# Performance work log

Measured on AMD Instinct MI355X. Metric: run time of the kernel, lower is better.

Reference implementation:

```python
import jax, jax.numpy as jnp
import numpy as np
from jax import lax

B, T, N, H, NC = 2, 8, 512, 64, 10
NEG = -1e9
LN_EPS = 1e-5


def _gatv2(x, mask, Wl, Wr, att, b):
    # GATv2Conv (PyG semantics, eval mode): e_ij = att . leaky_relu(Wr x_i + Wl x_j),
    # softmax over source nodes j with self-loops, out_i = sum_j alpha_ij * (Wl x_j).
    # x: (B, N, Fin); mask: (N, N) bool adjacency incl. self-loops; att: (heads, C).
    heads, C = att.shape
    Bn, Nn, _ = x.shape
    xl = (x @ Wl).reshape(Bn, Nn, heads, C)  # source transform
    xr = (x @ Wr).reshape(Bn, Nn, heads, C)  # target transform
    s = jax.nn.leaky_relu(xr[:, :, None] + xl[:, None, :], 0.2)  # (B, Ni, Nj, h, C)
    e = jnp.einsum('bijhc,hc->bijh', s, att)
    e = jnp.where(mask[None, :, :, None], e, NEG)
    alpha = jax.nn.softmax(e, axis=2)  # softmax over neighbors j
    out = jnp.einsum('bijh,bjhc->bihc', alpha, xl)
    return out.reshape(Bn, Nn, heads * C) + b


def _gru_layer(x, Wih, Whh, bih, bhh):
    # torch nn.GRU single layer, batch_first; x: (B, T, Hin)
    h0 = jnp.zeros((x.shape[0], Whh.shape[0]), x.dtype)
    def step(h, xt):
        gi = xt @ Wih + bih
        gh = h @ Whh + bhh
        ir, iz, inn = jnp.split(gi, 3, axis=-1)
        hr, hz, hn = jnp.split(gh, 3, axis=-1)
        r = jax.nn.sigmoid(ir + hr)
        z = jax.nn.sigmoid(iz + hz)
        n = jnp.tanh(inn + r * hn)
        hnew = (1.0 - z) * n + z * h
        return hnew, hnew
    _, ys = lax.scan(step, h0, jnp.swapaxes(x, 0, 1))
    return jnp.swapaxes(ys, 0, 1)


def setup_inputs() -> dict:
    key = jax.random.key(0)
    ks = jax.random.split(key, 20)
    def rn(i, shape, s=0.1):
        return jax.random.normal(ks[i], shape, jnp.float32) * s
    x_seq = jax.random.normal(ks[0], (B, T, N, 1), jnp.float32)
    a = jax.random.uniform(ks[1], (N, N))
    up = jnp.triu((a > 0.95).astype(jnp.float32), 1)
    static_adj = up + up.T  # sparse symmetric 0/1 static graph
    dyn_W = jax.random.normal(ks[2], (N, N), jnp.float32)
    reg_lambda = jnp.array([0.05], jnp.float32)
    return {
        'x_seq': x_seq, 'static_adj': static_adj, 'dyn_W': dyn_W, 'reg_lambda': reg_lambda,
        'g1_Wl': rn(3, (1, H)), 'g1_Wr': rn(4, (1, H)), 'g1_att': rn(5, (4, H // 4)), 'g1_b': jnp.zeros(H),
        'g2_Wl': rn(6, (H, H)), 'g2_Wr': rn(7, (H, H)), 'g2_att': rn(8, (1, H)), 'g2_b': jnp.zeros(H),
        'gru_Wih0': rn(9, (H, 3 * H)), 'gru_Whh0': rn(10, (H, 3 * H)), 'gru_bih0': jnp.zeros(3 * H), 'gru_bhh0': jnp.zeros(3 * H),
        'gru_Wih1': rn(11, (H, 3 * H)), 'gru_Whh1': rn(12, (H, 3 * H)), 'gru_bih1': jnp.zeros(3 * H), 'gru_bhh1': jnp.zeros(3 * H),
        'attn_W': rn(13, (H, 1)), 'attn_b': jnp.zeros(1),
        'cls_W1': rn(14, (H, H)), 'cls_b1': jnp.zeros(H), 'ln_g': jnp.ones(H), 'ln_b': jnp.zeros(H),
        'cls_W2': rn(15, (H, NC)), 'cls_b2': jnp.zeros(NC),
    }


def reference(x_seq, static_adj, dyn_W, reg_lambda,
              g1_Wl, g1_Wr, g1_att, g1_b, g2_Wl, g2_Wr, g2_att, g2_b,
              gru_Wih0, gru_Whh0, gru_bih0, gru_bhh0,
              gru_Wih1, gru_Whh1, gru_bih1, gru_bhh1,
              attn_W, attn_b, cls_W1, cls_b1, ln_g, ln_b, cls_W2, cls_b2):
    Bn, Tn, Nn, _ = x_seq.shape
    lam = jnp.maximum(reg_lambda[0], 0.01)
    t = jnp.arange(Tn, dtype=x_seq.dtype)
    gts = jnp.exp(-lam * t)  # gating values per timestep
    dyn = jax.nn.relu(dyn_W + dyn_W.T)
    fused = gts[:, None, None] * static_adj + (1.0 - gts)[:, None, None] * dyn  # (T, N, N)
    masks = (fused > 0) | jnp.eye(Nn, dtype=bool)[None]  # edge set + self-loops

    def step(carry, inp):
        xt, mask = inp  # xt: (B, N, 1)
        h = jax.nn.elu(_gatv2(xt, mask, g1_Wl, g1_Wr, g1_att, g1_b))
        h = jax.nn.elu(_gatv2(h, mask, g2_Wl, g2_Wr, g2_att, g2_b))
        return carry, h.mean(axis=1)  # (B, H) graph readout

    _, reps = lax.scan(step, 0.0, (jnp.swapaxes(x_seq, 0, 1), masks))
    h_seq = jnp.swapaxes(reps, 0, 1)  # (B, T, H)

    gru_out = _gru_layer(h_seq, gru_Wih0, gru_Whh0, gru_bih0, gru_bhh0)
    gru_out = _gru_layer(gru_out, gru_Wih1, gru_Whh1, gru_bih1, gru_bhh1)

    att_scores = jax.nn.softmax((gru_out @ attn_W + attn_b)[..., 0], axis=1)  # (B, T)
    final = jnp.einsum('bt,bth->bh', att_scores, gru_out)

    z = final @ cls_W1 + cls_b1
    mu = jnp.mean(z, axis=-1, keepdims=True)
    var = jnp.var(z, axis=-1, keepdims=True)
    z = (z - mu) / jnp.sqrt(var + LN_EPS) * ln_g + ln_b
    z = jax.nn.gelu(z, approximate=False)
    logits = z @ cls_W2 + cls_b2
    return logits, gts, att_scores
```

## Files before the change

### kernel.cpp

```cpp
#include <hip/hip_runtime.h>
#include <math.h>

#define BB 2
#define TT 8
#define NN 512
#define HH 64
#define NC 10

typedef unsigned char uchar;

__device__ __forceinline__ float elu1(float v){ return v > 0.f ? v : expm1f(v); }
__device__ __forceinline__ float sigm(float v){ return 1.f/(1.f+expf(-v)); }

__global__ __launch_bounds__(256) void k_mask(
    const float* __restrict__ dW, const float* __restrict__ sadj,
    uchar* __restrict__ M0, uchar* __restrict__ M1,
    float* __restrict__ hseq,
    const float* __restrict__ att1, const float* __restrict__ Wr1,
    const float* __restrict__ Wl1, float* __restrict__ AB,
    const float* __restrict__ Whh0, const float* __restrict__ Wih1,
    const float* __restrict__ Whh1, float4* __restrict__ WT4)
{
    __shared__ float tr[64][65];
    int bx = blockIdx.x, by = blockIdx.y;
    int tid = threadIdx.x;
    if (blockIdx.z == 1){
        int idx = (by*8 + bx)*256 + tid;
        if (idx < 3*4096){
            int m = idx >> 12, r = idx & 4095;
            int gg = r >> 6, k = r & 63;
            const float* W = (m == 0) ? Whh0 : (m == 1) ? Wih1 : Whh1;
            float4 o;
            o.x = W[k*192 + gg];
            o.y = W[k*192 + 64 + gg];
            o.z = W[k*192 + 128 + gg];
            o.w = 0.f;
            WT4[(size_t)m*4096 + r] = o;
        }
        return;
    }
    int i0 = by*64, j0 = bx*64;
    #pragma unroll
    for (int q = 0; q < 4; ++q){
        int r = (tid >> 4) + 16*q, c4 = tid & 15;
        float4 v = *(const float4*)&dW[(size_t)(j0+r)*NN + i0 + 4*c4];
        tr[r][4*c4+0] = v.x; tr[r][4*c4+1] = v.y;
        tr[r][4*c4+2] = v.z; tr[r][4*c4+3] = v.w;
    }
    __syncthreads();
    #pragma unroll
    for (int q = 0; q < 4; ++q){
        int row = (tid >> 4) + 16*q, c4 = tid & 15;
        int i = i0 + row, j = j0 + 4*c4;
        float4 d  = *(const float4*)&dW[(size_t)i*NN + j];
        float4 sa = *(const float4*)&sadj[(size_t)i*NN + j];
        uchar4 m0, m1;
        float dd0 = d.x + tr[4*c4+0][row];
        float dd1 = d.y + tr[4*c4+1][row];
        float dd2 = d.z + tr[4*c4+2][row];
        float dd3 = d.w + tr[4*c4+3][row];
        m0.x = (sa.x > 0.f) || (i == j+0);
        m0.y = (sa.y > 0.f) || (i == j+1);
        m0.z = (sa.z > 0.f) || (i == j+2);
        m0.w = (sa.w > 0.f) || (i == j+3);
        m1.x = m0.x || (dd0 > 0.f);
        m1.y = m0.y || (dd1 > 0.f);
        m1.z = m0.z || (dd2 > 0.f);
        m1.w = m0.w || (dd3 > 0.f);
        *(uchar4*)&M0[(size_t)i*NN + j] = m0;
        *(uchar4*)&M1[(size_t)i*NN + j] = m1;
    }
    int flat = (by*8 + bx)*256 + tid;
    if (flat < BB*TT*HH) hseq[flat] = 0.f;
    if (bx == 0 && by == 0 && tid < 8){
        int h = tid & 3;
        const float* W = (tid < 4) ? Wr1 : Wl1;
        float s = 0.f;
        for (int c = 0; c < 16; ++c) s += att1[h*16+c]*W[h*16+c];
        AB[tid] = s;
    }
}

__global__ __launch_bounds__(256) void k_gat1f(
    const float* __restrict__ x_seq, const uchar* __restrict__ M0,
    const uchar* __restrict__ M1,
    const float* __restrict__ Wl, const float* __restrict__ Wr,
    const float* __restrict__ att, const float* __restrict__ bias,
    const float* __restrict__ AB,
    const float* __restrict__ Wl2, const float* __restrict__ Wr2,
    const float* __restrict__ att2,
    float* __restrict__ xl2, float* __restrict__ xr2,
    float* __restrict__ ui, float* __restrict__ vj)
{
    __shared__ float x_s[NN];
    __shared__ float S_s[4][4];
    __shared__ float h_s[4][HH];
    __shared__ float Wl2_s[64*64];
    __shared__ float Wr2_s[64*64];
    int bt = blockIdx.y; int t = bt % TT;
    int i0 = blockIdx.x * 4;
    int tid = threadIdx.x;
    int il = tid >> 6, jl = tid & 63;
    int i = i0 + il;
    const uchar* M = t ? M1 : M0;
    ((float2*)x_s)[tid] = ((const float2*)(x_seq + bt*NN))[tid];
    #pragma unroll
    for (int q = 0; q < 4; ++q){
        int idx = q*256 + tid;
        ((float4*)Wl2_s)[idx] = ((const float4*)Wl2)[idx];
        ((float4*)Wr2_s)[idx] = ((const float4*)Wr2)[idx];
    }
    __syncthreads();
    float xi = x_s[i];
    const uchar* Mrow = M + (size_t)i*NN;
    float xj[8], msk[8];
    #pragma unroll
    for (int jj = 0; jj < 8; ++jj){
        int j = jj*64 + jl;
        xj[jj] = x_s[j];
        msk[jj] = Mrow[j] ? 1.f : 0.f;
    }
    float sw[4] = {0,0,0,0}, swx[4] = {0,0,0,0};
    for (int h = 0; h < 4; ++h){
        float acc[8] = {0,0,0,0,0,0,0,0};
        #pragma unroll
        for (int c = 0; c < 16; ++c){
            int hc = h*16 + c;
            float wl = Wl[hc];
            float q  = 0.4f * att[hc];
            float pr = xi * Wr[hc];
            #pragma unroll
            for (int jj = 0; jj < 8; ++jj){
                float s = fmaf(xj[jj], wl, pr);
                acc[jj] = fmaf(q, fabsf(s), acc[jj]);
            }
        }
        float lin = 0.6f * xi * AB[h];
        float al6 = 0.6f * AB[4+h];
        #pragma unroll
        for (int jj = 0; jj < 8; ++jj){
            float e = acc[jj] + fmaf(al6, xj[jj], lin);
            float w = msk[jj] * __expf(e);
            sw[h] += w;
            swx[h] = fmaf(w, xj[jj], swx[h]);
        }
    }
    #pragma unroll
    for (int off = 32; off; off >>= 1){
        #pragma unroll
        for (int h = 0; h < 4; ++h){
            sw[h]  += __shfl_down(sw[h],  off);
            swx[h] += __shfl_down(swx[h], off);
        }
    }
    if (jl == 0){
        #pragma unroll
        for (int h = 0; h < 4; ++h) S_s[il][h] = swx[h] / sw[h];
    }
    __syncthreads();
    {
        int hc = tid & 63, row = tid >> 6;
        float v = S_s[row][hc >> 4] * Wl[hc] + bias[hc];
        h_s[row][hc] = elu1(v);
    }
    __syncthreads();
    {
        int c = tid & 63, row = tid >> 6;
        float al = 0.f, ar = 0.f;
        #pragma unroll 8
        for (int k = 0; k < 64; ++k){
            float hv = h_s[row][k];
            al = fmaf(hv, Wl2_s[k*64 + c], al);
            ar = fmaf(hv, Wr2_s[k*64 + c], ar);
        }
        size_t ridx = (size_t)(bt*NN + i0 + row);
        xl2[ridx*HH + c] = al;
        xr2[ridx*HH + c] = ar;
        float a2 = att2[c];
        float pu = a2 * ar, pv = a2 * al;
        #pragma unroll
        for (int off = 32; off; off >>= 1){
            pu += __shfl_down(pu, off);
            pv += __shfl_down(pv, off);
        }
        if (c == 0){ ui[ridx] = pu; vj[ridx] = pv; }
    }
}

__global__ __launch_bounds__(256) void k_gat2(
    const float* __restrict__ xl2, const float* __restrict__ xr2,
    const uchar* __restrict__ M0, const uchar* __restrict__ M1,
    const float* __restrict__ att, const float* __restrict__ ui,
    const float* __restrict__ vj, const float* __restrict__ bias,
    float* __restrict__ hseq)
{
    __shared__ float xl_s[128][68];
    __shared__ float wT_s[128][36];
    __shared__ float xrT_s[64][36];
    __shared__ float v_s[128];
    __shared__ float u_s[32];
    __shared__ float z_s[32];
    __shared__ float q_s[64];

    int bt = blockIdx.y, t = bt & 7;
    int i0 = blockIdx.x * 32;
    int base = bt * NN;
    int tid = threadIdx.x;
    const uchar* M = t ? M1 : M0;

    #pragma unroll
    for (int q = 0; q < 2; ++q){
        int idx = q*256 + tid;
        int row = idx >> 4, c4 = idx & 15;
        float4 xv = ((const float4*)&xr2[(size_t)(base+i0+row)*HH])[c4];
        xrT_s[c4*4+0][row] = xv.x;
        xrT_s[c4*4+1][row] = xv.y;
        xrT_s[c4*4+2][row] = xv.z;
        xrT_s[c4*4+3][row] = xv.w;
    }
    if (tid < 32) u_s[tid] = ui[base + i0 + tid];
    if (tid < 64) q_s[tid] = 0.4f * att[tid];

    int ig = tid >> 5, jg = tid & 31;
    int wv = tid >> 6, ln = tid & 63;
    int ig2 = ln >> 3, cg2 = ln & 7;

    float zreg[4] = {0.f,0.f,0.f,0.f};
    float acc[4][8];
    #pragma unroll
    for (int a = 0; a < 4; ++a)
        #pragma unroll
        for (int r = 0; r < 8; ++r) acc[a][r] = 0.f;

    for (int tile = 0; tile < 4; ++tile){
        int j0 = tile * 128;
        __syncthreads();
        #pragma unroll
        for (int q = 0; q < 8; ++q){
            int idx = q*256 + tid;
            int row = idx >> 4, c4 = idx & 15;
            ((float4*)&xl_s[row][0])[c4] = ((const float4*)&xl2[(size_t)(base+j0+row)*HH])[c4];
        }
        if (tid < 128) v_s[tid] = vj[base + j0 + tid];
        __syncthreads();
        float e[4][4];
        {
            float u0 = 0.6f*u_s[ig*4+0], u1 = 0.6f*u_s[ig*4+1];
            float u2 = 0.6f*u_s[ig*4+2], u3 = 0.6f*u_s[ig*4+3];
            #pragma unroll
            for (int jj = 0; jj < 4; ++jj){
                float vv = 0.6f * v_s[jj*32 + jg];
                e[0][jj] = u0 + vv; e[1][jj] = u1 + vv;
                e[2][jj] = u2 + vv; e[3][jj] = u3 + vv;
            }
        }
        #pragma unroll 4
        for (int c4 = 0; c4 < 16; ++c4){
            float q4[4], xr4[4][4], xl4[4][4];
            *(float4*)q4 = *(const float4*)&q_s[c4*4];
            #pragma unroll
            for (int k = 0; k < 4; ++k)
                *(float4*)xr4[k] = *(const float4*)&xrT_s[c4*4+k][ig*4];
            #pragma unroll
            for (int jj = 0; jj < 4; ++jj)
                *(float4*)xl4[jj] = ((const float4*)&xl_s[jj*32+jg][0])[c4];
            #pragma unroll
            for (int jj = 0; jj < 4; ++jj)
                #pragma unroll
                for (int k = 0; k < 4; ++k){
                    float xc = xl4[jj][k];
                    #pragma unroll
                    for (int ii = 0; ii < 4; ++ii)
                        e[ii][jj] = fmaf(q4[k], fabsf(xr4[k][ii] + xc), e[ii][jj]);
                }
        }
        #pragma unroll
        for (int jj = 0; jj < 4; ++jj){
            int j = jj*32 + jg;
            float w0, w1, w2, w3;
            {
                uchar m0 = M[(size_t)(i0 + ig*4 + 0)*NN + j0 + j];
                uchar m1 = M[(size_t)(i0 + ig*4 + 1)*NN + j0 + j];
                uchar m2 = M[(size_t)(i0 + ig*4 + 2)*NN + j0 + j];
                uchar m3 = M[(size_t)(i0 + ig*4 + 3)*NN + j0 + j];
                w0 = m0 ? __expf(e[0][jj]) : 0.f;
                w1 = m1 ? __expf(e[1][jj]) : 0.f;
                w2 = m2 ? __expf(e[2][jj]) : 0.f;
                w3 = m3 ? __expf(e[3][jj]) : 0.f;
            }
            zreg[0] += w0; zreg[1] += w1; zreg[2] += w2; zreg[3] += w3;
            float4 wq; wq.x = w0; wq.y = w1; wq.z = w2; wq.w = w3;
            *(float4*)&wT_s[j][ig*4] = wq;
        }
        __syncthreads();
        #pragma unroll 4
        for (int jj = 0; jj < 32; ++jj){
            int j = wv*32 + jj;
            float w4[4], xa[8];
            *(float4*)w4      = *(const float4*)&wT_s[j][ig2*4];
            *(float4*)&xa[0]  = ((const float4*)&xl_s[j][0])[cg2*2+0];
            *(float4*)&xa[4]  = ((const float4*)&xl_s[j][0])[cg2*2+1];
            #pragma unroll
            for (int a = 0; a < 4; ++a)
                #pragma unroll
                for (int r = 0; r < 8; ++r)
                    acc[a][r] = fmaf(w4[a], xa[r], acc[a][r]);
        }
    }
    __syncthreads();
    #pragma unroll
    for (int off = 16; off; off >>= 1){
        #pragma unroll
        for (int ii = 0; ii < 4; ++ii) zreg[ii] += __shfl_down(zreg[ii], off, 32);
    }
    if (jg == 0){
        #pragma unroll
        for (int ii = 0; ii < 4; ++ii) z_s[ig*4+ii] = zreg[ii];
    }
    float* scratch = &xl_s[0][0];
    if (wv > 0){
        #pragma unroll
        for (int a = 0; a < 4; ++a)
            #pragma unroll
            for (int r = 0; r < 8; ++r)
                scratch[(a*8+r)*192 + (wv-1)*64 + ln] = acc[a][r];
    }
    __syncthreads();
    if (wv == 0){
        float pm[8];
        #pragma unroll
        for (int r = 0; r < 8; ++r) pm[r] = 0.f;
        #pragma unroll
        for (int a = 0; a < 4; ++a){
            float rz = 1.f / z_s[ig2*4 + a];
            #pragma unroll
            for (int r = 0; r < 8; ++r){
                float s = acc[a][r]
                        + scratch[(a*8+r)*192 +   0 + ln]
                        + scratch[(a*8+r)*192 +  64 + ln]
                        + scratch[(a*8+r)*192 + 128 + ln];
                float h = elu1(s*rz + bias[cg2*8 + r]);
                pm[r] += h;
            }
        }
        #pragma unroll
        for (int off = 32; off >= 8; off >>= 1){
            #pragma unroll
            for (int r = 0; r < 8; ++r) pm[r] += __shfl_down(pm[r], off);
        }
        if (ig2 == 0){
            #pragma unroll
            for (int r = 0; r < 8; ++r)
                atomicAdd(&hseq[bt*HH + cg2*8 + r], pm[r] * (1.f/(float)NN));
        }
    }
}

#define P4 65
__global__ __launch_bounds__(512) void k_gru2(
    const float* __restrict__ hseq, const float* __restrict__ Wih0,
    const float* __restrict__ bih0, const float4* __restrict__ WT4,
    const float* __restrict__ bhh0,
    const float* __restrict__ bih1, const float* __restrict__ bhh1,
    const float* __restrict__ lamp, const float* __restrict__ attn_W,
    const float* __restrict__ attn_b, const float* __restrict__ W1,
    const float* __restrict__ b1, const float* __restrict__ ln_g,
    const float* __restrict__ ln_b, const float* __restrict__ W2,
    const float* __restrict__ b2, float* __restrict__ out)
{
    __shared__ float4 WA[64*P4];
    __shared__ float4 WB[64*P4];
    __shared__ float gi_s[BB*TT*192];
    __shared__ float hs_s[BB*TT*HH];
    __shared__ float y_s[BB*TT*HH];
    __shared__ float sc_s[BB][TT], at_s[BB][TT];
    __shared__ float fin_s[BB][HH], z_s[BB][HH], g_s[BB][HH];
    __shared__ float mu_s[BB], iv_s[BB];
    int tid = threadIdx.x;
    int wave = tid >> 6, lane = tid & 63;
    for (int v = tid; v < 4096; v += 512){
        WA[(v >> 6)*P4 + (v & 63)] = WT4[v];
        WB[(v >> 6)*P4 + (v & 63)] = WT4[4096 + v];
    }
    for (int v = tid; v < BB*TT*HH; v += 512) hs_s[v] = hseq[v];
    __syncthreads();
    #pragma unroll
    for (int o = 0; o < 6; ++o){
        int idx = o*512 + tid;
        int b = idx / 192, g = idx % 192;
        float a = bih0[g];
        const float* hr = &hs_s[b*HH];
        #pragma unroll 8
        for (int k = 0; k < HH; ++k) a = fmaf(hr[k], Wih0[k*192 + g], a);
        gi_s[idx] = a;
    }
    __syncthreads();
    float y[TT];
    float g1r[TT], g1z[TT], g1n[TT];
    if (wave < 2){
        int b = wave;
        float bhr = bhh0[lane], bhz = bhh0[64+lane], bhn = bhh0[128+lane];
        float h = 0.f;
        for (int t = 0; t < TT; ++t){
            float ghr = bhr, ghz = bhz, ghn = bhn;
            #pragma unroll 16
            for (int k = 0; k < 64; ++k){
                float4 w4 = WA[lane*P4 + k];
                float hk = __shfl(h, k);
                ghr = fmaf(w4.x, hk, ghr);
                ghz = fmaf(w4.y, hk, ghz);
                ghn = fmaf(w4.z, hk, ghn);
            }
            const float* gi = &gi_s[(b*TT + t)*192];
            float r = sigm(gi[lane] + ghr);
            float z = sigm(gi[64+lane] + ghz);
            float n = tanhf(gi[128+lane] + r*ghn);
            h = (1.f - z)*n + z*h;
            y[t] = h;
        }
        float bi1r = bih1[lane], bi1z = bih1[64+lane], bi1n = bih1[128+lane];
        #pragma unroll
        for (int t = 0; t < TT; ++t){ g1r[t] = bi1r; g1z[t] = bi1z; g1n[t] = bi1n; }
        #pragma unroll 8
        for (int k = 0; k < 64; ++k){
            float4 w4 = WB[lane*P4 + k];
            #pragma unroll
            for (int t = 0; t < TT; ++t){
                float yk = __shfl(y[t], k);
                g1r[t] = fmaf(w4.x, yk, g1r[t]);
                g1z[t] = fmaf(w4.y, yk, g1z[t]);
                g1n[t] = fmaf(w4.z, yk, g1n[t]);
            }
        }
    }
    __syncthreads();
    if (wave >= 2){
        for (int v = tid - 128; v < 4096; v += 384)
            WA[(v >> 6)*P4 + (v & 63)] = WT4[2*4096 + v];
    }
    __syncthreads();
    if (wave < 2){
        int b = wave;
        float bhr = bhh1[lane], bhz = bhh1[64+lane], bhn = bhh1[128+lane];
        float h = 0.f;
        for (int t = 0; t < TT; ++t){
            float ghr = bhr, ghz = bhz, ghn = bhn;
            #pragma unroll 16
            for (int k = 0; k < 64; ++k){
                float4 w4 = WA[lane*P4 + k];
                float hk = __shfl(h, k);
                ghr = fmaf(w4.x, hk, ghr);
                ghz = fmaf(w4.y, hk, ghz);
                ghn = fmaf(w4.z, hk, ghn);
            }
            float r = sigm(g1r[t] + ghr);
            float z = sigm(g1z[t] + ghz);
            float n = tanhf(g1n[t] + r*ghn);
            h = (1.f - z)*n + z*h;
            y_s[(b*TT + t)*HH + lane] = h;
        }
    }
    __syncthreads();
    float lam = fmaxf(lamp[0], 0.01f);
    if (tid < TT) out[BB*NC + tid] = expf(-lam*(float)tid);
    if (tid < BB*TT){
        int bb = tid >> 3, t = tid & 7;
        float s = attn_b[0];
        const float* r = &y_s[(bb*TT+t)*HH];
        for (int h = 0; h < HH; ++h) s += r[h]*attn_W[h];
        sc_s[bb][t] = s;
    }
    __syncthreads();
    if (tid < BB){
        float mx = -INFINITY;
        for (int t = 0; t < TT; ++t) mx = fmaxf(mx, sc_s[tid][t]);
        float se = 0.f;
        for (int t = 0; t < TT; ++t){ float w = expf(sc_s[tid][t]-mx); at_s[tid][t] = w; se += w; }
        for (int t = 0; t < TT; ++t){
            at_s[tid][t] /= se;
            out[BB*NC + TT + tid*TT + t] = at_s[tid][t];
        }
    }
    __syncthreads();
    if (tid < BB*HH){
        int bb = tid >> 6, h = tid & 63;
        float a = 0.f;
        for (int t = 0; t < TT; ++t) a += at_s[bb][t]*y_s[(bb*TT+t)*HH + h];
        fin_s[bb][h] = a;
    }
    __syncthreads();
    if (tid < BB*HH){
        int bb = tid >> 6, h = tid & 63;
        float a = b1[h];
        for (int k = 0; k < HH; ++k) a += fin_s[bb][k]*W1[k*HH+h];
        z_s[bb][h] = a;
    }
    __syncthreads();
    if (tid < BB){
        float mu = 0.f;
        for (int h = 0; h < HH; ++h) mu += z_s[tid][h];
        mu *= (1.f/HH);
        float v = 0.f;
        for (int h = 0; h < HH; ++h){ float d = z_s[tid][h]-mu; v += d*d; }
        v *= (1.f/HH);
        mu_s[tid] = mu; iv_s[tid] = 1.f/sqrtf(v + 1e-5f);
    }
    __syncthreads();
    if (tid < BB*HH){
        int bb = tid >> 6, h = tid & 63;
        float zn = (z_s[bb][h]-mu_s[bb])*iv_s[bb]*ln_g[h] + ln_b[h];
        g_s[bb][h] = 0.5f*zn*(1.f + erff(zn*0.70710678118654752f));
    }
    __syncthreads();
    if (tid < BB*NC){
        int bb = tid / NC, c = tid % NC;
        float a = b2[c];
        for (int k = 0; k < HH; ++k) a += g_s[bb][k]*W2[k*NC+c];
        out[bb*NC + c] = a;
    }
}

extern "C" void kernel_launch(void* const* d_in, const int* in_sizes, int n_in,
                              void* d_out, int out_size, void* d_ws, size_t ws_size,
                              hipStream_t stream)
{
    const float* x_seq = (const float*)d_in[0];
    const float* sadj  = (const float*)d_in[1];
    const float* dynW  = (const float*)d_in[2];
    const float* lamp  = (const float*)d_in[3];
    const float* g1_Wl = (const float*)d_in[4];
    const float* g1_Wr = (const float*)d_in[5];
    const float* g1_att= (const float*)d_in[6];
    const float* g1_b  = (const float*)d_in[7];
    const float* g2_Wl = (const float*)d_in[8];
    const float* g2_Wr = (const float*)d_in[9];
    const float* g2_att= (const float*)d_in[10];
    const float* g2_b  = (const float*)d_in[11];
    const float* Wih0  = (const float*)d_in[12];
    const float* Whh0  = (const float*)d_in[13];
    const float* bih0  = (const float*)d_in[14];
    const float* bhh0  = (const float*)d_in[15];
    const float* Wih1  = (const float*)d_in[16];
    const float* Whh1  = (const float*)d_in[17];
    const float* bih1  = (const float*)d_in[18];
    const float* bhh1  = (const float*)d_in[19];
    const float* attnW = (const float*)d_in[20];
    const float* attnb = (const float*)d_in[21];
    const float* W1    = (const float*)d_in[22];
    const float* b1    = (const float*)d_in[23];
    const float* lng   = (const float*)d_in[24];
    const float* lnb   = (const float*)d_in[25];
    const float* W2    = (const float*)d_in[26];
    const float* b2    = (const float*)d_in[27];
    float* out = (float*)d_out;

    const int RWS = BB*TT*NN*HH;
    uchar* M0 = (uchar*)d_ws;
    uchar* M1 = M0 + (size_t)NN*NN;
    float* fb = (float*)(M1 + (size_t)NN*NN);
    float* AB   = fb;
    float* ui   = AB   + 16;
    float* vj   = ui   + BB*TT*NN;
    float* xl2  = vj   + BB*TT*NN;
    float* xr2  = xl2  + RWS;
    float* hseq = xr2  + RWS;
    float4* WT4 = (float4*)(hseq + BB*TT*HH);

    k_mask <<<dim3(8,8,2), 256, 0, stream>>>(dynW, sadj, M0, M1, hseq, g1_att, g1_Wr, g1_Wl, AB,
                                             Whh0, Wih1, Whh1, WT4);
    k_gat1f<<<dim3(NN/4, BB*TT), 256, 0, stream>>>(x_seq, M0, M1, g1_Wl, g1_Wr, g1_att, g1_b, AB,
                                                   g2_Wl, g2_Wr, g2_att, xl2, xr2, ui, vj);
    k_gat2 <<<dim3(NN/32, BB*TT), 256, 0, stream>>>(xl2, xr2, M0, M1, g2_att, ui, vj, g2_b, hseq);
    k_gru2 <<<1, 512, 0, stream>>>(hseq, Wih0, bih0, WT4, bhh0, bih1, bhh1,
                                   lamp, attnW, attnb, W1, b1, lng, lnb, W2, b2, out);
}
```

Measured before the change: 229.5 us.

## Widen GAT layer-2 block to 512 threads with 256-node tiles

The k_gat2 block grows to 512 threads (8 waves) and processes source nodes in two tiles of 256 instead of four of 128, so there are fewer tile loads and barriers. The transposed xr shared tile and the staged u/att values are removed. Each wave now owns 4 target rows and reads its xr rows and att from global memory (via cache) with wave-uniform addressing. The cross-wave reduction now sums 7 partial accumulators instead of 3. Shared memory use roughly doubles (~106KB), which limits residency to one block per CU, and the grid is still only 256 blocks.

```diff
diff --git a/kernel.cpp b/kernel.cpp
--- a/kernel.cpp
+++ b/kernel.cpp
@@ -187,20 +187,17 @@
     }
 }
 
-__global__ __launch_bounds__(256) void k_gat2(
+__global__ __launch_bounds__(512) void k_gat2(
     const float* __restrict__ xl2, const float* __restrict__ xr2,
     const uchar* __restrict__ M0, const uchar* __restrict__ M1,
     const float* __restrict__ att, const float* __restrict__ ui,
     const float* __restrict__ vj, const float* __restrict__ bias,
     float* __restrict__ hseq)
 {
-    __shared__ float xl_s[128][68];
-    __shared__ float wT_s[128][36];
-    __shared__ float xrT_s[64][36];
-    __shared__ float v_s[128];
-    __shared__ float u_s[32];
+    __shared__ float xl_s[256][68];
+    __shared__ float wT_s[256][36];
+    __shared__ float v_s[256];
     __shared__ float z_s[32];
-    __shared__ float q_s[64];
 
     int bt = blockIdx.y, t = bt & 7;
     int i0 = blockIdx.x * 32;
@@ -208,22 +205,19 @@
     int tid = threadIdx.x;
     const uchar* M = t ? M1 : M0;
 
-    #pragma unroll
-    for (int q = 0; q < 2; ++q){
-        int idx = q*256 + tid;
-        int row = idx >> 4, c4 = idx & 15;
-        float4 xv = ((const float4*)&xr2[(size_t)(base+i0+row)*HH])[c4];
-        xrT_s[c4*4+0][row] = xv.x;
-        xrT_s[c4*4+1][row] = xv.y;
-        xrT_s[c4*4+2][row] = xv.z;
-        xrT_s[c4*4+3][row] = xv.w;
-    }
-    if (tid < 32) u_s[tid] = ui[base + i0 + tid];
-    if (tid < 64) q_s[tid] = 0.4f * att[tid];
-
-    int ig = tid >> 5, jg = tid & 31;
-    int wv = tid >> 6, ln = tid & 63;
+    int ig = __builtin_amdgcn_readfirstlane(tid >> 6);
+    int jg = tid & 63;
+    int ln = jg;
     int ig2 = ln >> 3, cg2 = ln & 7;
+
+    const float* xrp0 = xr2 + (size_t)(base + i0 + ig*4 + 0)*HH;
+    const float* xrp1 = xr2 + (size_t)(base + i0 + ig*4 + 1)*HH;
+    const float* xrp2 = xr2 + (size_t)(base + i0 + ig*4 + 2)*HH;
+    const float* xrp3 = xr2 + (size_t)(base + i0 + ig*4 + 3)*HH;
+    float u0 = 0.6f*ui[base + i0 + ig*4 + 0];
+    float u1 = 0.6f*ui[base + i0 + ig*4 + 1];
+    float u2 = 0.6f*ui[base + i0 + ig*4 + 2];
+    float u3 = 0.6f*ui[base + i0 + ig*4 + 3];
 
     float zreg[4] = {0.f,0.f,0.f,0.f};
     float acc[4][8];
@@ -232,62 +226,56 @@
         #pragma unroll
         for (int r = 0; r < 8; ++r) acc[a][r] = 0.f;
 
-    for (int tile = 0; tile < 4; ++tile){
-        int j0 = tile * 128;
+    for (int tile = 0; tile < 2; ++tile){
+        int j0 = tile * 256;
         __syncthreads();
         #pragma unroll
         for (int q = 0; q < 8; ++q){
-            int idx = q*256 + tid;
+            int idx = q*512 + tid;
             int row = idx >> 4, c4 = idx & 15;
             ((float4*)&xl_s[row][0])[c4] = ((const float4*)&xl2[(size_t)(base+j0+row)*HH])[c4];
         }
-        if (tid < 128) v_s[tid] = vj[base + j0 + tid];
+        if (tid < 256) v_s[tid] = vj[base + j0 + tid];
         __syncthreads();
         float e[4][4];
-        {
-            float u0 = 0.6f*u_s[ig*4+0], u1 = 0.6f*u_s[ig*4+1];
-            float u2 = 0.6f*u_s[ig*4+2], u3 = 0.6f*u_s[ig*4+3];
-            #pragma unroll
-            for (int jj = 0; jj < 4; ++jj){
-                float vv = 0.6f * v_s[jj*32 + jg];
-                e[0][jj] = u0 + vv; e[1][jj] = u1 + vv;
-                e[2][jj] = u2 + vv; e[3][jj] = u3 + vv;
-            }
+        #pragma unroll
+        for (int jj = 0; jj < 4; ++jj){
+            float vv = 0.6f * v_s[jj*64 + jg];
+            e[0][jj] = u0 + vv; e[1][jj] = u1 + vv;
+            e[2][jj] = u2 + vv; e[3][jj] = u3 + vv;
         }
         #pragma unroll 4
         for (int c4 = 0; c4 < 16; ++c4){
-            float q4[4], xr4[4][4], xl4[4][4];
-            *(float4*)q4 = *(const float4*)&q_s[c4*4];
-            #pragma unroll
-            for (int k = 0; k < 4; ++k)
-                *(float4*)xr4[k] = *(const float4*)&xrT_s[c4*4+k][ig*4];
+            float4 a4 = *(const float4*)&att[c4*4];
+            float qk[4];
+            qk[0] = 0.4f*a4.x; qk[1] = 0.4f*a4.y; qk[2] = 0.4f*a4.z; qk[3] = 0.4f*a4.w;
+            float rr[4][4];
+            *(float4*)rr[0] = *(const float4*)&xrp0[c4*4];
+            *(float4*)rr[1] = *(const float4*)&xrp1[c4*4];
+            *(float4*)rr[2] = *(const float4*)&xrp2[c4*4];
+            *(float4*)rr[3] = *(const float4*)&xrp3[c4*4];
+            float xlv[4][4];
             #pragma unroll
             for (int jj = 0; jj < 4; ++jj)
-                *(float4*)xl4[jj] = ((const float4*)&xl_s[jj*32+jg][0])[c4];
+                *(float4*)xlv[jj] = ((const float4*)&xl_s[jj*64+jg][0])[c4];
             #pragma unroll
             for (int jj = 0; jj < 4; ++jj)
                 #pragma unroll
                 for (int k = 0; k < 4; ++k){
-                    float xc = xl4[jj][k];
+                    float xc = xlv[jj][k];
                     #pragma unroll
                     for (int ii = 0; ii < 4; ++ii)
-                        e[ii][jj] = fmaf(q4[k], fabsf(xr4[k][ii] + xc), e[ii][jj]);
+                        e[ii][jj] = fmaf(qk[k], fabsf(rr[ii][k] + xc), e[ii][jj]);
                 }
         }
         #pragma unroll
         for (int jj = 0; jj < 4; ++jj){
-            int j = jj*32 + jg;
-            float w0, w1, w2, w3;
-            {
-                uchar m0 = M[(size_t)(i0 + ig*4 + 0)*NN + j0 + j];
-                uchar m1 = M[(size_t)(i0 + ig*4 + 1)*NN + j0 + j];
-                uchar m2 = M[(size_t)(i0 + ig*4 + 2)*NN + j0 + j];
-                uchar m3 = M[(size_t)(i0 + ig*4 + 3)*NN + j0 + j];
-                w0 = m0 ? __expf(e[0][jj]) : 0.f;
-                w1 = m1 ? __expf(e[1][jj]) : 0.f;
-                w2 = m2 ? __expf(e[2][jj]) : 0.f;
-                w3 = m3 ? __expf(e[3][jj]) : 0.f;
-            }
+            int j = jj*64 + jg;
+            const uchar* mp = &M[(size_t)(i0 + ig*4)*NN + j0 + j];
+            float w0 = mp[0]      ? __expf(e[0][jj]) : 0.f;
+            float w1 = mp[NN]     ? __expf(e[1][jj]) : 0.f;
+            float w2 = mp[2*NN]   ? __expf(e[2][jj]) : 0.f;
+            float w3 = mp[3*NN]   ? __expf(e[3][jj]) : 0.f;
             zreg[0] += w0; zreg[1] += w1; zreg[2] += w2; zreg[3] += w3;
             float4 wq; wq.x = w0; wq.y = w1; wq.z = w2; wq.w = w3;
             *(float4*)&wT_s[j][ig*4] = wq;
@@ -295,7 +283,7 @@
         __syncthreads();
         #pragma unroll 4
         for (int jj = 0; jj < 32; ++jj){
-            int j = wv*32 + jj;
+            int j = ig*32 + jj;
             float w4[4], xa[8];
             *(float4*)w4      = *(const float4*)&wT_s[j][ig2*4];
             *(float4*)&xa[0]  = ((const float4*)&xl_s[j][0])[cg2*2+0];
@@ -309,24 +297,24 @@
     }
     __syncthreads();
     #pragma unroll
-    for (int off = 16; off; off >>= 1){
-        #pragma unroll
-        for (int ii = 0; ii < 4; ++ii) zreg[ii] += __shfl_down(zreg[ii], off, 32);
+    for (int off = 32; off; off >>= 1){
+        #pragma unroll
+        for (int ii = 0; ii < 4; ++ii) zreg[ii] += __shfl_down(zreg[ii], off);
     }
     if (jg == 0){
         #pragma unroll
         for (int ii = 0; ii < 4; ++ii) z_s[ig*4+ii] = zreg[ii];
     }
     float* scratch = &xl_s[0][0];
-    if (wv > 0){
+    if (ig > 0){
         #pragma unroll
         for (int a = 0; a < 4; ++a)
             #pragma unroll
             for (int r = 0; r < 8; ++r)
-                scratch[(a*8+r)*192 + (wv-1)*64 + ln] = acc[a][r];
-    }
-    __syncthreads();
-    if (wv == 0){
+                scratch[(a*8+r)*448 + (ig-1)*64 + ln] = acc[a][r];
+    }
+    __syncthreads();
+    if (ig == 0){
         float pm[8];
         #pragma unroll
         for (int r = 0; r < 8; ++r) pm[r] = 0.f;
@@ -335,10 +323,10 @@
             float rz = 1.f / z_s[ig2*4 + a];
             #pragma unroll
             for (int r = 0; r < 8; ++r){
-                float s = acc[a][r]
-                        + scratch[(a*8+r)*192 +   0 + ln]
-                        + scratch[(a*8+r)*192 +  64 + ln]
-                        + scratch[(a*8+r)*192 + 128 + ln];
+                float s = acc[a][r];
+                #pragma unroll
+                for (int w = 0; w < 7; ++w)
+                    s += scratch[(a*8+r)*448 + w*64 + ln];
                 float h = elu1(s*rz + bias[cg2*8 + r]);
                 pm[r] += h;
             }
@@ -570,7 +558,7 @@
                                              Whh0, Wih1, Whh1, WT4);
     k_gat1f<<<dim3(NN/4, BB*TT), 256, 0, stream>>>(x_seq, M0, M1, g1_Wl, g1_Wr, g1_att, g1_b, AB,
                                                    g2_Wl, g2_Wr, g2_att, xl2, xr2, ui, vj);
-    k_gat2 <<<dim3(NN/32, BB*TT), 256, 0, stream>>>(xl2, xr2, M0, M1, g2_att, ui, vj, g2_b, hseq);
+    k_gat2 <<<dim3(NN/32, BB*TT), 512, 0, stream>>>(xl2, xr2, M0, M1, g2_att, ui, vj, g2_b, hseq);
     k_gru2 <<<1, 512, 0, stream>>>(hseq, Wih0, bih0, WT4, bhh0, bih1, bhh1,
                                    lamp, attnW, attnb, W1, b1, lng, lnb, W2, b2, out);
 }
```

Result: faster. 222.8 us (-2.9%).
